# Kernel tuning notes

Measured on AMD Instinct MI355X. Metric: run time of the kernel, lower is better.

## Reference

```python
import jax, jax.numpy as jnp
import numpy as np

B, L, C = 8, 4096, 256
H = 8            # num_heads
D = C // H       # head_dim = 32
CHUNK = 128


def _build_slopes(n):
    # ALiBi slopes for power-of-2 n: 2^(-8/n * (i+1)); cast fp16 like the torch module
    s = np.array([2.0 ** (-(8.0 / n) * (i + 1)) for i in range(n)], dtype=np.float32)
    return jnp.asarray(s.astype(np.float16).astype(np.float32))  # [H]


def setup_inputs() -> dict:
    key = jax.random.key(0)
    ks = jax.random.split(key, 6)
    x = jax.random.normal(ks[0], (B, L, C), dtype=jnp.float32)
    rel_pos = jax.random.normal(ks[1], (1, L, C), dtype=jnp.float32) * 0.02  # trunc_normal std=0.02
    qkv_w = jax.random.normal(ks[2], (3 * C, C), dtype=jnp.float32) * (C ** -0.5)
    q_gamma = jnp.ones((H, 1, D), dtype=jnp.float32) / (D ** 0.5)
    k_gamma = jnp.ones((H, 1, D), dtype=jnp.float32) / (D ** 0.5)
    proj_w = jax.random.normal(ks[3], (C, C), dtype=jnp.float32) * (C ** -0.5)
    proj_b = jnp.zeros((C,), dtype=jnp.float32)
    return {"x": x, "rel_pos": rel_pos, "qkv_w": qkv_w, "q_gamma": q_gamma,
            "k_gamma": k_gamma, "proj_w": proj_w, "proj_b": proj_b}


def _rms_norm(t, gamma):
    # t: [B,H,L,D]; gamma: [H,1,D]. F.normalize(dim=-1) then * sqrt(D) * gamma
    n = jnp.sqrt(jnp.sum(t * t, axis=-1, keepdims=True))
    t = t / jnp.maximum(n, 1e-12)
    return t * (D ** 0.5) * gamma[None]


def _lightning_attn(q, k, v, slopes):
    # q,k,v: [B,H,L,D]; slopes: [H]. o_t = sum_{s<=t} exp(-slope*(t-s)) (q_t.k_s) v_s
    nc = L // CHUNK
    c = CHUNK
    qc = q.reshape(B, H, nc, c, D)
    kc = k.reshape(B, H, nc, c, D)
    vc = v.reshape(B, H, nc, c, D)

    idx = jnp.arange(c, dtype=jnp.float32)
    diff = idx[:, None] - idx[None, :]                       # [c,c]
    s = slopes[:, None, None]                                # [H,1,1]
    mask = jnp.where(diff >= 0, jnp.exp(-s * diff), 0.0)     # [H,c,c]

    # intra-chunk: [B,H,nc,c,c]
    scores = jnp.einsum("bhncd,bhnmd->bhncm", qc, kc) * mask[None, :, None]
    o_intra = jnp.einsum("bhncm,bhnmd->bhncd", scores, vc)

    # inter-chunk recurrence over decayed KV state [B,H,D,D]
    q_decay = jnp.exp(-slopes[:, None] * idx[None, :])[None, :, :, None]        # [1,H,c,1]
    k_decay = jnp.exp(-slopes[:, None] * (c - idx[None, :]))[None, :, :, None]  # [1,H,c,1]
    blk_decay = jnp.exp(-slopes * c)[:, None, None]                             # [H,1,1]

    def step(kv, inp):
        qi, ki, vi = inp                                   # each [B,H,c,D]
        o = jnp.einsum("bhcd,bhde->bhce", qi * q_decay, kv)
        kv = blk_decay * kv + jnp.einsum("bhcd,bhce->bhde", ki * k_decay, vi)
        return kv, o

    kv0 = jnp.zeros((B, H, D, D), dtype=q.dtype)
    qs = jnp.moveaxis(qc, 2, 0)  # [nc,B,H,c,D]
    ks_ = jnp.moveaxis(kc, 2, 0)
    vs = jnp.moveaxis(vc, 2, 0)
    _, o_inter = jax.lax.scan(step, kv0, (qs, ks_, vs))    # [nc,B,H,c,D]
    o_inter = jnp.moveaxis(o_inter, 0, 2)                  # [B,H,nc,c,D]

    return (o_intra + o_inter).reshape(B, H, L, D)


def reference(x, rel_pos, qkv_w, q_gamma, k_gamma, proj_w, proj_b):
    slopes = _build_slopes(H)
    h = x + rel_pos                                        # [B,L,C]
    qkv = h @ qkv_w.T                                      # [B,L,3C]
    qkv = qkv.reshape(B, L, 3, H, D).transpose(2, 0, 3, 1, 4)  # [3,B,H,L,D]
    q, k, v = qkv[0], qkv[1], qkv[2]
    q = q * (D ** -0.5)            # no-op through normalize, kept for fidelity
    q = _rms_norm(q, q_gamma)
    k = _rms_norm(k, k_gamma)
    o = _lightning_attn(q, k, v, slopes)                   # [B,H,L,D]
    o = o.transpose(0, 2, 1, 3).reshape(B, L, C)
    return o @ proj_w.T + proj_b
```

## Files before the change

### kernel.cpp

```cpp
#include <hip/hip_runtime.h>
#include <hip/hip_bf16.h>

#define B_ 8
#define L_ 4096
#define C_ 256
#define H_ 8
#define D_ 32
#define CHUNK_ 128
#define NC_ 32
#define M_ (B_*L_)

typedef _Float16 f16x8 __attribute__((ext_vector_type(8)));
typedef _Float16 f16x4 __attribute__((ext_vector_type(4)));
typedef float    f32x4 __attribute__((ext_vector_type(4)));

#define GLOAD_LDS16(g, l) __builtin_amdgcn_global_load_lds( \
    (const __attribute__((address_space(1))) unsigned int*)(g), \
    (__attribute__((address_space(3))) unsigned int*)(l), 16, 0, 0)

__global__ __launch_bounds__(256) void k_prep(
    const float* __restrict__ x, const float* __restrict__ rel,
    const float* __restrict__ qw, const float* __restrict__ pw,
    _Float16* __restrict__ h, _Float16* __restrict__ qwb, _Float16* __restrict__ pwb)
{
    const int bx = blockIdx.x;
    if (bx < 4096) {
        const int i = (bx * 256 + threadIdx.x) * 8;
        float4 x0 = *(const float4*)(x + i);
        float4 x1 = *(const float4*)(x + i + 4);
        const int ri = i & (L_ * C_ - 1);
        float4 r0 = *(const float4*)(rel + ri);
        float4 r1 = *(const float4*)(rel + ri + 4);
        f16x8 o = { (_Float16)(x0.x + r0.x), (_Float16)(x0.y + r0.y),
                    (_Float16)(x0.z + r0.z), (_Float16)(x0.w + r0.w),
                    (_Float16)(x1.x + r1.x), (_Float16)(x1.y + r1.y),
                    (_Float16)(x1.z + r1.z), (_Float16)(x1.w + r1.w) };
        *(f16x8*)(h + i) = o;
    } else {
        const int i = ((bx - 4096) * 256 + threadIdx.x) * 4;
        const float* src; _Float16* dst; int off;
        if (i < 768 * 256) { src = qw; dst = qwb; off = i; }
        else               { src = pw; dst = pwb; off = i - 768 * 256; }
        float4 v = *(const float4*)(src + off);
        f16x4 o = { (_Float16)v.x, (_Float16)v.y, (_Float16)v.z, (_Float16)v.w };
        *(f16x4*)(dst + off) = o;
    }
}

__global__ __launch_bounds__(256) void k_qkv_gemm(
    const _Float16* __restrict__ A, const _Float16* __restrict__ Bw,
    const float* __restrict__ qg, const float* __restrict__ kg,
    _Float16* __restrict__ Qg, _Float16* __restrict__ Kg, _Float16* __restrict__ Vtg)
{
    __shared__ __align__(16) char smem[34816];
    _Float16* As = (_Float16*)smem;
    _Float16* Bs = As + 128 * 32;
    _Float16* Ws = (_Float16*)smem;

    const int blk = blockIdx.x;
    const int xcd = blk & 7;
    const int t   = blk >> 3;
    const int by  = xcd * 32 + (t & 31);
    const int bx  = t >> 5;
    const int m0 = by * 128;
    const int n0 = bx * 128;

    const int tid = threadIdx.x;
    const int wv = tid >> 6, ln = tid & 63;
    const int lr = ln >> 2, lc = (ln & 3) * 8;
    const int wm = (wv >> 1) * 64, wn = (wv & 1) * 64;
    const int fr = ln & 15, fk = (ln >> 4) * 8;

    f32x4 acc[4][4] = {};
    const _Float16* ga = A  + (size_t)(m0 + wv * 16 + lr) * 256 + lc;
    const _Float16* gb = Bw + (size_t)(n0 + wv * 16 + lr) * 256 + lc;

    for (int k0 = 0; k0 < 256; k0 += 32) {
        GLOAD_LDS16(ga + k0,            As + (wv * 16) * 32);
        GLOAD_LDS16(ga + k0 + 64 * 256, As + (64 + wv * 16) * 32);
        GLOAD_LDS16(gb + k0,            Bs + (wv * 16) * 32);
        GLOAD_LDS16(gb + k0 + 64 * 256, Bs + (64 + wv * 16) * 32);
        __syncthreads();
        f16x8 af[4], bf[4];
#pragma unroll
        for (int i = 0; i < 4; ++i)
            af[i] = *(const f16x8*)(As + (wm + i * 16 + fr) * 32 + fk);
#pragma unroll
        for (int j = 0; j < 4; ++j)
            bf[j] = *(const f16x8*)(Bs + (wn + j * 16 + fr) * 32 + fk);
#pragma unroll
        for (int i = 0; i < 4; ++i)
#pragma unroll
            for (int j = 0; j < 4; ++j)
                acc[i][j] = __builtin_amdgcn_mfma_f32_16x16x32_f16(
                    af[i], bf[j], acc[i][j], 0, 0, 0);
        __syncthreads();
    }

    const int cr = (ln >> 4) * 4, cc = ln & 15;
    const int kind = n0 >> 8;
    const int col0 = (n0 & 255) + wn;
    const int bb = m0 >> 12, l00 = m0 & 4095;
    const int hbase = (n0 & 255) >> 5;

    if (kind < 2) {
        const float* gsrc = kind ? kg : qg;
        float gma[2][2];
#pragma unroll
        for (int jp = 0; jp < 2; ++jp)
#pragma unroll
            for (int jj = 0; jj < 2; ++jj)
                gma[jp][jj] = gsrc[((col0 >> 5) + jp) * 32 + jj * 16 + cc];
#pragma unroll
        for (int i = 0; i < 4; ++i)
#pragma unroll
            for (int r = 0; r < 4; ++r) {
                const int irow = wm + i * 16 + cr + r;
#pragma unroll
                for (int jp = 0; jp < 2; ++jp) {
                    const float a0 = acc[i][jp * 2][r];
                    const float a1 = acc[i][jp * 2 + 1][r];
                    float ss = a0 * a0 + a1 * a1;
                    ss += __shfl_xor(ss, 1);
                    ss += __shfl_xor(ss, 2);
                    ss += __shfl_xor(ss, 4);
                    ss += __shfl_xor(ss, 8);
                    const float sc = 5.656854249492381f / fmaxf(sqrtf(ss), 1e-12f);
                    Ws[irow * 136 + wn + jp * 32 + cc]      = (_Float16)(a0 * sc * gma[jp][0]);
                    Ws[irow * 136 + wn + jp * 32 + 16 + cc] = (_Float16)(a1 * sc * gma[jp][1]);
                }
            }
        __syncthreads();
        _Float16* P = kind ? Kg : Qg;
#pragma unroll
        for (int kk = 0; kk < 8; ++kk) {
            const int c = kk * 256 + tid;
            const int hh = c >> 9;
            const int rr = (c >> 2) & 127;
            const int part = (c & 3) * 8;
            f16x8 v8 = *(const f16x8*)(Ws + rr * 136 + hh * 32 + part);
            *(f16x8*)(P + ((size_t)(bb * 8 + hbase + hh) * 4096 + l00 + rr) * 32 + part) = v8;
        }
    } else {
#pragma unroll
        for (int i = 0; i < 4; ++i)
#pragma unroll
            for (int j = 0; j < 4; ++j) {
                const int colL = wn + j * 16 + cc;
                const int row0 = wm + i * 16 + cr;
                f16x4 v4 = { (_Float16)acc[i][j][0], (_Float16)acc[i][j][1],
                             (_Float16)acc[i][j][2], (_Float16)acc[i][j][3] };
                *(f16x4*)(Ws + colL * 132 + row0) = v4;
            }
        __syncthreads();
#pragma unroll
        for (int kk = 0; kk < 8; ++kk) {
            const int q = kk * 256 + tid;
            const int c = q >> 4;
            const int seg = q & 15;
            const int col = (n0 & 255) + c;
            const int hh = col >> 5, e = col & 31;
            f16x8 v8 = *(const f16x8*)(Ws + c * 132 + seg * 8);
            *(f16x8*)(Vtg + ((size_t)(bb * 8 + hh) * 32 + e) * 4096 + l00 + seg * 8) = v8;
        }
    }
}

__global__ __launch_bounds__(64) void k_chunk_kv(
    const _Float16* __restrict__ Kg, const _Float16* __restrict__ Vtg,
    float* __restrict__ kvbuf)
{
    __shared__ _Float16 Vp[32 * 136];
    __shared__ _Float16 Kp[32 * 136];
    const int blk = blockIdx.x;
    const int n  = blk & 31;
    const int bh = blk >> 5;
    const int h  = bh & 7;
    const float sl2 = exp2f(-(float)(h + 1)) * 1.44269504f;
    const int ln = threadIdx.x;
    const _Float16* Kc = Kg  + ((size_t)bh * 4096 + n * CHUNK_) * 32;
    const _Float16* Vc = Vtg + (size_t)bh * 32 * 4096 + n * CHUNK_;
#pragma unroll
    for (int i = 0; i < 8; ++i) {
        const int flat = i * 64 + ln;
        const int e = flat >> 4, seg = flat & 15;
        f16x8 v8 = *(const f16x8*)(Vc + (size_t)e * 4096 + seg * 8);
        *(f16x8*)(Vp + e * 136 + seg * 8) = v8;
        const int pos = flat >> 2, d0 = (flat & 3) * 8;
        f16x8 k8 = *(const f16x8*)(Kc + flat * 8);
#pragma unroll
        for (int j = 0; j < 8; ++j) Kp[(d0 + j) * 136 + pos] = k8[j];
    }
    __syncthreads();
    const int fr = ln & 15, fk = (ln >> 4) * 8;
    const float r = exp2f(sl2);
    float rj[8];
    rj[0] = 1.f;
#pragma unroll
    for (int j = 1; j < 8; ++j) rj[j] = rj[j - 1] * r;
    f32x4 acc[2][2] = {};
    for (int k0 = 0; k0 < 128; k0 += 32) {
        const float e0 = exp2f(-sl2 * (float)(CHUNK_ - (k0 + fk)));
        f16x8 av[2], bd[2];
#pragma unroll
        for (int i = 0; i < 2; ++i)
            av[i] = *(const f16x8*)(Vp + (i * 16 + fr) * 136 + k0 + fk);
#pragma unroll
        for (int jt = 0; jt < 2; ++jt) {
            f16x8 kraw = *(const f16x8*)(Kp + (jt * 16 + fr) * 136 + k0 + fk);
            f16x8 kb;
#pragma unroll
            for (int j = 0; j < 8; ++j)
                kb[j] = (_Float16)((float)kraw[j] * (e0 * rj[j]));
            bd[jt] = kb;
        }
#pragma unroll
        for (int i = 0; i < 2; ++i)
#pragma unroll
            for (int jt = 0; jt < 2; ++jt)
                acc[i][jt] = __builtin_amdgcn_mfma_f32_16x16x32_f16(
                    av[i], bd[jt], acc[i][jt], 0, 0, 0);
    }
    const int cr = (ln >> 4) * 4, cc = ln & 15;
    float* outp = kvbuf + (size_t)blk * 1024;
#pragma unroll
    for (int i = 0; i < 2; ++i)
#pragma unroll
        for (int jt = 0; jt < 2; ++jt)
#pragma unroll
            for (int rr = 0; rr < 4; ++rr)
                outp[(i * 16 + cr + rr) * 32 + jt * 16 + cc] = acc[i][jt][rr];
}

__global__ __launch_bounds__(64) void k_scan(float* __restrict__ kvbuf)
{
    const int blk = blockIdx.x;
    const int bh  = blk >> 2;
    const int grp = blk & 3;
    const int tid = threadIdx.x;
    const float slope = exp2f(-(float)((bh & 7) + 1));
    const float bd = __expf(-slope * (float)CHUNK_);
    float4 st = {0.f, 0.f, 0.f, 0.f};
    float4* base = (float4*)(kvbuf + (size_t)bh * NC_ * 1024) + grp * 64 + tid;
#pragma unroll
    for (int g = 0; g < 4; ++g) {
        float4 tmp[8];
#pragma unroll
        for (int k = 0; k < 8; ++k) tmp[k] = base[(g * 8 + k) * 256];
#pragma unroll
        for (int k = 0; k < 8; ++k) {
            base[(g * 8 + k) * 256] = st;
            st.x = bd * st.x + tmp[k].x;
            st.y = bd * st.y + tmp[k].y;
            st.z = bd * st.z + tmp[k].z;
            st.w = bd * st.w + tmp[k].w;
        }
    }
}

__global__ __launch_bounds__(256) void k_attn(
    const _Float16* __restrict__ Qg, const _Float16* __restrict__ Kg,
    const _Float16* __restrict__ Vtg, const float* __restrict__ kvbuf,
    _Float16* __restrict__ attnp)
{
    __shared__ __align__(16) _Float16 Ss[128 * 144];
    const int blk = blockIdx.x;
    const int n  = blk & 31;
    const int bh = blk >> 5;
    const int h  = bh & 7;
    const float sl2 = exp2f(-(float)(h + 1)) * 1.44269504f;
    const int tid = threadIdx.x;
    const int wv = tid >> 6, ln = tid & 63;
    const int fr = ln & 15, fk = (ln >> 4) * 8;
    const int cr = (ln >> 4) * 4, cc = ln & 15;
    const int rb0 = wv;
    const int rb1 = 7 - wv;

    const _Float16* Qc = Qg + ((size_t)bh * 4096 + n * CHUNK_) * 32;
    const _Float16* Kc = Kg + ((size_t)bh * 4096 + n * CHUNK_) * 32;
    const _Float16* Vc = Vtg + (size_t)bh * 32 * 4096 + n * CHUNK_;
    const float* kvp = kvbuf + (size_t)blk * 1024;

    f16x8 aq0 = *(const f16x8*)(Qc + (rb0 * 16 + fr) * 32 + fk);
    f16x8 aq1 = *(const f16x8*)(Qc + (rb1 * 16 + fr) * 32 + fk);

    f32x4 iacc[2][2] = {};
#pragma unroll
    for (int ct = 0; ct < 2; ++ct) {
        const float* kp = kvp + (ct * 16 + fr) * 32 + fk;
        f32x4 k0 = *(const f32x4*)kp;
        f32x4 k1 = *(const f32x4*)(kp + 4);
        f16x8 bkv = { (_Float16)k0[0], (_Float16)k0[1], (_Float16)k0[2], (_Float16)k0[3],
                      (_Float16)k1[0], (_Float16)k1[1], (_Float16)k1[2], (_Float16)k1[3] };
        iacc[0][ct] = __builtin_amdgcn_mfma_f32_16x16x32_f16(aq0, bkv, iacc[0][ct], 0, 0, 0);
        iacc[1][ct] = __builtin_amdgcn_mfma_f32_16x16x32_f16(aq1, bkv, iacc[1][ct], 0, 0, 0);
    }

    const float c1  = exp2f(-sl2);
    const float r16 = exp2f(sl2 * 16.f);
    float er0[4], er1[4];
    {
        float e0 = exp2f(-sl2 * (float)(rb0 * 16 + cr));
        float e1 = exp2f(-sl2 * (float)(rb1 * 16 + cr));
#pragma unroll
        for (int r = 0; r < 4; ++r) { er0[r] = e0; er1[r] = e1; e0 *= c1; e1 *= c1; }
    }

    float ej = exp2f(sl2 * (float)cc);
#pragma unroll
    for (int j = 0; j < 8; ++j) {
        if (j <= rb1) {
            f16x8 bk = *(const f16x8*)(Kc + (j * 16 + fr) * 32 + fk);
            f32x4 z = {};
            f32x4 s1 = __builtin_amdgcn_mfma_f32_16x16x32_f16(aq1, bk, z, 0, 0, 0);
            f32x4 s0 = {};
            if (j <= rb0)
                s0 = __builtin_amdgcn_mfma_f32_16x16x32_f16(aq0, bk, z, 0, 0, 0);
            const int jcol = j * 16 + cc;
#pragma unroll
            for (int r = 0; r < 4; ++r) {
                const int i1 = rb1 * 16 + cr + r;
                const float w1 = (jcol <= i1) ? ej * er1[r] : 0.f;
                Ss[i1 * 144 + jcol] = (_Float16)(s1[r] * w1);
                if (j <= rb0) {
                    const int i0 = rb0 * 16 + cr + r;
                    const float w0 = (jcol <= i0) ? ej * er0[r] : 0.f;
                    Ss[i0 * 144 + jcol] = (_Float16)(s0[r] * w0);
                }
            }
        }
        ej *= r16;
    }

    {
        const int rbe = (wv & 1) ? rb1 : rb0;
#pragma unroll
        for (int r = 0; r < 4; ++r)
            Ss[(rbe * 16 + cr + r) * 144 + (rbe + 1) * 16 + cc] = (_Float16)0;
    }

    const int km0 = (rb0 >> 1) + 1;
    const int km1 = (rb1 >> 1) + 1;
    f32x4 oacc[2][2] = {};
#pragma unroll
    for (int k = 0; k < 4; ++k) {
        if (k < km1) {
            f16x8 bv0 = *(const f16x8*)(Vc + (size_t)(fr) * 4096 + k * 32 + fk);
            f16x8 bv1 = *(const f16x8*)(Vc + (size_t)(16 + fr) * 4096 + k * 32 + fk);
            f16x8 as1 = *(const f16x8*)(Ss + (rb1 * 16 + fr) * 144 + k * 32 + fk);
            oacc[1][0] = __builtin_amdgcn_mfma_f32_16x16x32_f16(as1, bv0, oacc[1][0], 0, 0, 0);
            oacc[1][1] = __builtin_amdgcn_mfma_f32_16x16x32_f16(as1, bv1, oacc[1][1], 0, 0, 0);
            if (k < km0) {
                f16x8 as0 = *(const f16x8*)(Ss + (rb0 * 16 + fr) * 144 + k * 32 + fk);
                oacc[0][0] = __builtin_amdgcn_mfma_f32_16x16x32_f16(as0, bv0, oacc[0][0], 0, 0, 0);
                oacc[0][1] = __builtin_amdgcn_mfma_f32_16x16x32_f16(as0, bv1, oacc[0][1], 0, 0, 0);
            }
        }
    }

#pragma unroll
    for (int r = 0; r < 4; ++r) {
        const int i0 = rb0 * 16 + cr + r;
        const int i1 = rb1 * 16 + cr + r;
        Ss[i0 * 144 + cc]      = (_Float16)(oacc[0][0][r] + er0[r] * iacc[0][0][r]);
        Ss[i0 * 144 + 16 + cc] = (_Float16)(oacc[0][1][r] + er0[r] * iacc[0][1][r]);
        Ss[i1 * 144 + cc]      = (_Float16)(oacc[1][0][r] + er1[r] * iacc[1][0][r]);
        Ss[i1 * 144 + 16 + cc] = (_Float16)(oacc[1][1][r] + er1[r] * iacc[1][1][r]);
    }
    _Float16* abase = attnp + ((size_t)bh * 4096 + n * CHUNK_) * 32;
    {
        const int rloc = ln >> 2, part = (ln & 3) * 8;
        const int i0 = rb0 * 16 + rloc;
        const int i1 = rb1 * 16 + rloc;
        f16x8 v0 = *(const f16x8*)(Ss + i0 * 144 + part);
        f16x8 v1 = *(const f16x8*)(Ss + i1 * 144 + part);
        *(f16x8*)(abase + i0 * 32 + part) = v0;
        *(f16x8*)(abase + i1 * 32 + part) = v1;
    }
}

__global__ __launch_bounds__(256) void k_proj_gemm(
    const _Float16* __restrict__ attnp, const _Float16* __restrict__ Bw,
    const float* __restrict__ bias, float* __restrict__ Cc)
{
    __shared__ _Float16 As[128 * 32];
    __shared__ _Float16 Bs[128 * 32];
    const int blk = blockIdx.x;
    const int xcd = blk & 7;
    const int t   = blk >> 3;
    const int m0 = (xcd * 32 + (t & 31)) * 128;
    const int n0 = (t >> 5) * 128;

    const int tid = threadIdx.x;
    const int wv = tid >> 6, ln = tid & 63;
    const int lr = ln >> 2;
    const int lc = (ln & 3) * 8;
    const int wm = (wv >> 1) * 64;
    const int wn = (wv & 1) * 64;
    const int fr = ln & 15;
    const int fk = (ln >> 4) * 8;

    f32x4 acc[4][4] = {};
    const int gmrow = m0 + wv * 16 + lr;
    const _Float16* ga = attnp +
        ((size_t)(gmrow >> 12) * 8 * 4096 + (gmrow & 4095)) * 32 + lc;
    const _Float16* gb = Bw + (size_t)(n0 + wv * 16 + lr) * 256 + lc;

    for (int k0 = 0; k0 < 256; k0 += 32) {
        const size_t hoff = (size_t)(k0 >> 5) * (4096 * 32);
        GLOAD_LDS16(ga + hoff,           As + (wv * 16) * 32);
        GLOAD_LDS16(ga + hoff + 64 * 32, As + (64 + wv * 16) * 32);
        GLOAD_LDS16(gb + k0,             Bs + (wv * 16) * 32);
        GLOAD_LDS16(gb + k0 + 64 * 256,  Bs + (64 + wv * 16) * 32);
        __syncthreads();
        f16x8 af[4], bf[4];
#pragma unroll
        for (int i = 0; i < 4; ++i)
            af[i] = *(const f16x8*)(As + (wm + i * 16 + fr) * 32 + fk);
#pragma unroll
        for (int j = 0; j < 4; ++j)
            bf[j] = *(const f16x8*)(Bs + (wn + j * 16 + fr) * 32 + fk);
#pragma unroll
        for (int i = 0; i < 4; ++i)
#pragma unroll
            for (int j = 0; j < 4; ++j)
                acc[i][j] = __builtin_amdgcn_mfma_f32_16x16x32_f16(
                    af[i], bf[j], acc[i][j], 0, 0, 0);
        __syncthreads();
    }
    const int cr = (ln >> 4) * 4;
    const int cc = ln & 15;
#pragma unroll
    for (int i = 0; i < 4; ++i)
#pragma unroll
        for (int j = 0; j < 4; ++j) {
            const int row = m0 + wm + i * 16 + cr;
            const int col = n0 + wn + j * 16 + cc;
            float* cp = Cc + (size_t)row * 256 + col;
            const float bb = bias[col];
#pragma unroll
            for (int r = 0; r < 4; ++r) cp[(size_t)r * 256] = acc[i][j][r] + bb;
        }
}

extern "C" void kernel_launch(void* const* d_in, const int* in_sizes, int n_in,
                              void* d_out, int out_size, void* d_ws, size_t ws_size,
                              hipStream_t stream)
{
    const float* x     = (const float*)d_in[0];
    const float* rel   = (const float*)d_in[1];
    const float* qkv_w = (const float*)d_in[2];
    const float* qg    = (const float*)d_in[3];
    const float* kg    = (const float*)d_in[4];
    const float* pw    = (const float*)d_in[5];
    const float* pb    = (const float*)d_in[6];
    float* out = (float*)d_out;
    char* wsb = (char*)d_ws;

    float*    kvb   = (float*)wsb;
    _Float16* Qg    = (_Float16*)(wsb + ((size_t)8  << 20));
    _Float16* Kg    = (_Float16*)(wsb + ((size_t)24 << 20));
    _Float16* Vtg   = (_Float16*)(wsb + ((size_t)40 << 20));
    _Float16* attnp = (_Float16*)(wsb + ((size_t)56 << 20));
    _Float16* hb    = (_Float16*)(wsb + ((size_t)72 << 20));
    _Float16* qwb   = (_Float16*)(wsb + ((size_t)88 << 20));
    _Float16* pwb   = (_Float16*)(wsb + ((size_t)89 << 20));

    k_prep<<<4352, 256, 0, stream>>>(x, rel, qkv_w, pw, hb, qwb, pwb);
    k_qkv_gemm<<<1536, 256, 0, stream>>>(hb, qwb, qg, kg, Qg, Kg, Vtg);
    k_chunk_kv<<<2048, 64, 0, stream>>>(Kg, Vtg, kvb);
    k_scan<<<256, 64, 0, stream>>>(kvb);
    k_attn<<<2048, 256, 0, stream>>>(Qg, Kg, Vtg, kvb, attnp);
    k_proj_gemm<<<512, 256, 0, stream>>>(attnp, pwb, pb, out);
}
```

Before: 171.6 us.

## Fuse chunk KV state computation and inter-chunk scan into one kernel

Replaces the per-chunk KV kernel and the separate scan kernel with one kernel per (batch, head). Its 8 waves each compute a chunk's decayed K^T V via MFMA and stage the result in LDS, then all threads run the recurrence and write prefix states in fp16. This removes a launch and the fp32 round trip of the KV buffer, and halves the state read in the attention kernel. In exchange only 64 blocks are launched, so much of the GPU sits idle. K is also read with strided scalar global loads instead of LDS-staged transposes.

```diff
diff --git a/kernel.cpp b/kernel.cpp
--- a/kernel.cpp
+++ b/kernel.cpp
@@ -12,6 +12,7 @@
 
 typedef _Float16 f16x8 __attribute__((ext_vector_type(8)));
 typedef _Float16 f16x4 __attribute__((ext_vector_type(4)));
+typedef _Float16 f16x2 __attribute__((ext_vector_type(2)));
 typedef float    f32x4 __attribute__((ext_vector_type(4)));
 
 #define GLOAD_LDS16(g, l) __builtin_amdgcn_global_load_lds( \
@@ -166,101 +167,82 @@
     }
 }
 
-__global__ __launch_bounds__(64) void k_chunk_kv(
+__global__ __launch_bounds__(512) void k_kv(
     const _Float16* __restrict__ Kg, const _Float16* __restrict__ Vtg,
-    float* __restrict__ kvbuf)
-{
-    __shared__ _Float16 Vp[32 * 136];
-    __shared__ _Float16 Kp[32 * 136];
-    const int blk = blockIdx.x;
-    const int n  = blk & 31;
-    const int bh = blk >> 5;
+    _Float16* __restrict__ kvst)
+{
+    __shared__ float kvraw[8 * 1056];
+    const int bh = blockIdx.x;
     const int h  = bh & 7;
     const float sl2 = exp2f(-(float)(h + 1)) * 1.44269504f;
-    const int ln = threadIdx.x;
-    const _Float16* Kc = Kg  + ((size_t)bh * 4096 + n * CHUNK_) * 32;
-    const _Float16* Vc = Vtg + (size_t)bh * 32 * 4096 + n * CHUNK_;
-#pragma unroll
-    for (int i = 0; i < 8; ++i) {
-        const int flat = i * 64 + ln;
-        const int e = flat >> 4, seg = flat & 15;
-        f16x8 v8 = *(const f16x8*)(Vc + (size_t)e * 4096 + seg * 8);
-        *(f16x8*)(Vp + e * 136 + seg * 8) = v8;
-        const int pos = flat >> 2, d0 = (flat & 3) * 8;
-        f16x8 k8 = *(const f16x8*)(Kc + flat * 8);
-#pragma unroll
-        for (int j = 0; j < 8; ++j) Kp[(d0 + j) * 136 + pos] = k8[j];
-    }
-    __syncthreads();
+    const float bdc = exp2f(-sl2 * 128.f);
+    const int tid = threadIdx.x;
+    const int wv = tid >> 6, ln = tid & 63;
     const int fr = ln & 15, fk = (ln >> 4) * 8;
+    const int cr = (ln >> 4) * 4, cc = ln & 15;
     const float r = exp2f(sl2);
     float rj[8];
     rj[0] = 1.f;
 #pragma unroll
     for (int j = 1; j < 8; ++j) rj[j] = rj[j - 1] * r;
-    f32x4 acc[2][2] = {};
-    for (int k0 = 0; k0 < 128; k0 += 32) {
-        const float e0 = exp2f(-sl2 * (float)(CHUNK_ - (k0 + fk)));
-        f16x8 av[2], bd[2];
+
+    const int f0 = tid * 2;
+    const int a0 = f0 + (f0 >> 5);
+    float s0 = 0.f, s1 = 0.f;
+
+    for (int p = 0; p < 4; ++p) {
+        const int n = p * 8 + wv;
+        const _Float16* Kc = Kg  + ((size_t)bh * 4096 + n * CHUNK_) * 32;
+        const _Float16* Vc = Vtg + (size_t)bh * 32 * 4096 + n * CHUNK_;
+        f32x4 acc[2][2] = {};
+#pragma unroll
+        for (int k0 = 0; k0 < 128; k0 += 32) {
+            const float e0 = exp2f(-sl2 * (float)(CHUNK_ - (k0 + fk)));
+            f16x8 av[2], bkd[2];
+#pragma unroll
+            for (int i = 0; i < 2; ++i)
+                av[i] = *(const f16x8*)(Vc + (size_t)(i * 16 + fr) * 4096 + k0 + fk);
+#pragma unroll
+            for (int jt = 0; jt < 2; ++jt) {
+                f16x8 kb;
+#pragma unroll
+                for (int j = 0; j < 8; ++j)
+                    kb[j] = (_Float16)((float)Kc[(size_t)(k0 + fk + j) * 32 + jt * 16 + fr]
+                                       * (e0 * rj[j]));
+                bkd[jt] = kb;
+            }
+#pragma unroll
+            for (int i = 0; i < 2; ++i)
+#pragma unroll
+                for (int jt = 0; jt < 2; ++jt)
+                    acc[i][jt] = __builtin_amdgcn_mfma_f32_16x16x32_f16(
+                        av[i], bkd[jt], acc[i][jt], 0, 0, 0);
+        }
+        float* outp = kvraw + wv * 1056;
 #pragma unroll
         for (int i = 0; i < 2; ++i)
-            av[i] = *(const f16x8*)(Vp + (i * 16 + fr) * 136 + k0 + fk);
-#pragma unroll
-        for (int jt = 0; jt < 2; ++jt) {
-            f16x8 kraw = *(const f16x8*)(Kp + (jt * 16 + fr) * 136 + k0 + fk);
-            f16x8 kb;
-#pragma unroll
-            for (int j = 0; j < 8; ++j)
-                kb[j] = (_Float16)((float)kraw[j] * (e0 * rj[j]));
-            bd[jt] = kb;
-        }
-#pragma unroll
-        for (int i = 0; i < 2; ++i)
 #pragma unroll
             for (int jt = 0; jt < 2; ++jt)
-                acc[i][jt] = __builtin_amdgcn_mfma_f32_16x16x32_f16(
-                    av[i], bd[jt], acc[i][jt], 0, 0, 0);
-    }
-    const int cr = (ln >> 4) * 4, cc = ln & 15;
-    float* outp = kvbuf + (size_t)blk * 1024;
-#pragma unroll
-    for (int i = 0; i < 2; ++i)
-#pragma unroll
-        for (int jt = 0; jt < 2; ++jt)
-#pragma unroll
-            for (int rr = 0; rr < 4; ++rr)
-                outp[(i * 16 + cr + rr) * 32 + jt * 16 + cc] = acc[i][jt][rr];
-}
-
-__global__ __launch_bounds__(64) void k_scan(float* __restrict__ kvbuf)
-{
-    const int blk = blockIdx.x;
-    const int bh  = blk >> 2;
-    const int grp = blk & 3;
-    const int tid = threadIdx.x;
-    const float slope = exp2f(-(float)((bh & 7) + 1));
-    const float bd = __expf(-slope * (float)CHUNK_);
-    float4 st = {0.f, 0.f, 0.f, 0.f};
-    float4* base = (float4*)(kvbuf + (size_t)bh * NC_ * 1024) + grp * 64 + tid;
-#pragma unroll
-    for (int g = 0; g < 4; ++g) {
-        float4 tmp[8];
-#pragma unroll
-        for (int k = 0; k < 8; ++k) tmp[k] = base[(g * 8 + k) * 256];
-#pragma unroll
-        for (int k = 0; k < 8; ++k) {
-            base[(g * 8 + k) * 256] = st;
-            st.x = bd * st.x + tmp[k].x;
-            st.y = bd * st.y + tmp[k].y;
-            st.z = bd * st.z + tmp[k].z;
-            st.w = bd * st.w + tmp[k].w;
-        }
+#pragma unroll
+                for (int rr = 0; rr < 4; ++rr)
+                    outp[(i * 16 + cr + rr) * 33 + jt * 16 + cc] = acc[i][jt][rr];
+        __syncthreads();
+        _Float16* kb2 = kvst + (((size_t)bh * 32 + p * 8) * 1024) + f0;
+#pragma unroll
+        for (int m = 0; m < 8; ++m) {
+            f16x2 o = { (_Float16)s0, (_Float16)s1 };
+            *(f16x2*)(kb2 + (size_t)m * 1024) = o;
+            const float* rp = kvraw + m * 1056 + a0;
+            s0 = bdc * s0 + rp[0];
+            s1 = bdc * s1 + rp[1];
+        }
+        if (p < 3) __syncthreads();
     }
 }
 
 __global__ __launch_bounds__(256) void k_attn(
     const _Float16* __restrict__ Qg, const _Float16* __restrict__ Kg,
-    const _Float16* __restrict__ Vtg, const float* __restrict__ kvbuf,
+    const _Float16* __restrict__ Vtg, const _Float16* __restrict__ kvst,
     _Float16* __restrict__ attnp)
 {
     __shared__ __align__(16) _Float16 Ss[128 * 144];
@@ -279,7 +261,7 @@
     const _Float16* Qc = Qg + ((size_t)bh * 4096 + n * CHUNK_) * 32;
     const _Float16* Kc = Kg + ((size_t)bh * 4096 + n * CHUNK_) * 32;
     const _Float16* Vc = Vtg + (size_t)bh * 32 * 4096 + n * CHUNK_;
-    const float* kvp = kvbuf + (size_t)blk * 1024;
+    const _Float16* kvp = kvst + (size_t)blk * 1024;
 
     f16x8 aq0 = *(const f16x8*)(Qc + (rb0 * 16 + fr) * 32 + fk);
     f16x8 aq1 = *(const f16x8*)(Qc + (rb1 * 16 + fr) * 32 + fk);
@@ -287,11 +269,7 @@
     f32x4 iacc[2][2] = {};
 #pragma unroll
     for (int ct = 0; ct < 2; ++ct) {
-        const float* kp = kvp + (ct * 16 + fr) * 32 + fk;
-        f32x4 k0 = *(const f32x4*)kp;
-        f32x4 k1 = *(const f32x4*)(kp + 4);
-        f16x8 bkv = { (_Float16)k0[0], (_Float16)k0[1], (_Float16)k0[2], (_Float16)k0[3],
-                      (_Float16)k1[0], (_Float16)k1[1], (_Float16)k1[2], (_Float16)k1[3] };
+        f16x8 bkv = *(const f16x8*)(kvp + (ct * 16 + fr) * 32 + fk);
         iacc[0][ct] = __builtin_amdgcn_mfma_f32_16x16x32_f16(aq0, bkv, iacc[0][ct], 0, 0, 0);
         iacc[1][ct] = __builtin_amdgcn_mfma_f32_16x16x32_f16(aq1, bkv, iacc[1][ct], 0, 0, 0);
     }
@@ -457,7 +435,7 @@
     float* out = (float*)d_out;
     char* wsb = (char*)d_ws;
 
-    float*    kvb   = (float*)wsb;
+    _Float16* kvst  = (_Float16*)wsb;
     _Float16* Qg    = (_Float16*)(wsb + ((size_t)8  << 20));
     _Float16* Kg    = (_Float16*)(wsb + ((size_t)24 << 20));
     _Float16* Vtg   = (_Float16*)(wsb + ((size_t)40 << 20));
@@ -468,8 +446,7 @@
 
     k_prep<<<4352, 256, 0, stream>>>(x, rel, qkv_w, pw, hb, qwb, pwb);
     k_qkv_gemm<<<1536, 256, 0, stream>>>(hb, qwb, qg, kg, Qg, Kg, Vtg);
-    k_chunk_kv<<<2048, 64, 0, stream>>>(Kg, Vtg, kvb);
-    k_scan<<<256, 64, 0, stream>>>(kvb);
-    k_attn<<<2048, 256, 0, stream>>>(Qg, Kg, Vtg, kvb, attnp);
+    k_kv<<<64, 512, 0, stream>>>(Kg, Vtg, kvst);
+    k_attn<<<2048, 256, 0, stream>>>(Qg, Kg, Vtg, kvst, attnp);
     k_proj_gemm<<<512, 256, 0, stream>>>(attnp, pwb, pb, out);
 }
```

Measured after the change: 174.8 us. No clear change (+1.9%).
